# Kernel optimization log

Measured on AMD Instinct MI355X. Metric: run time of the kernel, lower is better.

## Reference

```python
import jax, jax.numpy as jnp
import numpy as np

B, N, D, H = 4, 256, 32, 512

def setup_inputs() -> dict:
    key = jax.random.key(0)
    ks = jax.random.split(key, 6)
    z = jax.random.normal(ks[0], (B, N, D), dtype=jnp.float32)
    motif_mask = (jax.random.uniform(ks[1], (B, N)) > 0.5).astype(jnp.float32)
    residue_mask = jnp.ones((B, N), dtype=jnp.float32)
    # Linear weights stored as (in, out); scaled like torch default init
    W1 = jax.random.normal(ks[2], (D * D, H), dtype=jnp.float32) / np.sqrt(D * D)
    b1 = jnp.zeros((H,), dtype=jnp.float32)
    W2 = jax.random.normal(ks[3], (H, H // 2), dtype=jnp.float32) / np.sqrt(H)
    b2 = jnp.zeros((H // 2,), dtype=jnp.float32)
    W3 = jax.random.normal(ks[4], (H // 2, 1), dtype=jnp.float32) / np.sqrt(H // 2)
    b3 = jnp.zeros((1,), dtype=jnp.float32)
    return {"z": z, "motif_mask": motif_mask, "residue_mask": residue_mask,
            "W1": W1, "b1": b1, "W2": W2, "b2": b2, "W3": W3, "b3": b3}

def reference(z, motif_mask, residue_mask, W1, b1, W2, b2, W3, b3):
    # kron[b,i,j, a*D+c] = z[b,i,a] * z[b,j,c]; first Linear on kron is the
    # bilinear form z_i^T W1_h z_j -- compute via two matmuls, never
    # materializing the (B,N,N,D^2) tensor.
    d = z.shape[-1]
    W1r = W1.reshape(d, d, -1)                      # (D, D, H); axis0 = z_i dim, axis1 = z_j dim
    tmp = jnp.einsum('bia,ach->bihc', z, W1r)        # (B, N, H, D)
    h1 = jax.nn.relu(jnp.einsum('bihc,bjc->bijh', tmp, z) + b1)  # (B, N, N, H)
    h2 = jax.nn.relu(jnp.einsum('bijh,hk->bijk', h1, W2) + b2)   # (B, N, N, H/2)
    contact_logits = (jnp.einsum('bijk,ko->bijo', h2, W3) + b3)[..., 0]  # (B, N, N)
    outer_mask = motif_mask[:, None, :] * motif_mask[:, :, None]
    contact_logits = contact_logits * outer_mask
    contact_map = jax.nn.sigmoid(contact_logits)
    return (contact_map, contact_logits)
```

## Files before the change

kernel.cpp:

```cpp
#include <hip/hip_runtime.h>
#include <hip/hip_bf16.h>
#include <cstdint>
#include <cstddef>

#define NB 4
#define NN 256
#define DD 32
#define HH 512

typedef __attribute__((ext_vector_type(8))) short short8;
typedef __attribute__((ext_vector_type(4))) float f32x4;
typedef __attribute__((ext_vector_type(16))) float f32x16;

static __device__ __forceinline__ unsigned cvtpk(float a, float b) {
  unsigned r;
  asm("v_cvt_pk_bf16_f32 %0, %1, %2" : "=v"(r) : "v"(a), "v"(b));
  return r;
}
static __device__ __forceinline__ unsigned short f2bf1(float a) {
  return (unsigned short)(cvtpk(a, 0.f) & 0xffffu);
}

static __device__ __forceinline__ short8 pack8(float4 a0, float4 a1) {
  union { unsigned u[4]; short8 s; } r;
  r.u[0] = cvtpk(a0.x, a0.y); r.u[1] = cvtpk(a0.z, a0.w);
  r.u[2] = cvtpk(a1.x, a1.y); r.u[3] = cvtpk(a1.z, a1.w);
  return r.s;
}

__global__ __launch_bounds__(256) void prep(const float* __restrict__ z,
                                            const float* __restrict__ W1,
                                            const float* __restrict__ W2,
                                            unsigned short* __restrict__ W2F,
                                            unsigned short* __restrict__ Tall) {
  const int blk = blockIdx.x;
  const int tid = threadIdx.x;
  if (blk < 512) {
    __shared__ unsigned short w1s[16384];
    const int nblk = blk >> 4, mgrp = blk & 15;
    const int bibase = mgrp * 64;

    #pragma unroll
    for (int r = 0; r < 16; ++r) {
      int task = r * 256 + tid;
      int row = task >> 2;
      int hq = task & 3;
      float4 v = *(const float4*)(W1 + (size_t)row * 512 + nblk * 16 + hq * 4);
      int a = row >> 5, c = row & 31;
      int quad = a >> 3, e = a & 7;
      float hv[4] = {v.x, v.y, v.z, v.w};
      #pragma unroll
      for (int vv = 0; vv < 4; ++vv) {
        int hl = hq * 4 + vv;
        int nl = hl * 32 + c;
        int w2 = nl >> 7, r7 = nl & 127;
        int l16 = r7 >> 3, nt = r7 & 7;
        w1s[((w2 * 8 + nt) * 64 + quad * 16 + l16) * 8 + e] = f2bf1(hv[vv]);
      }
    }
    __syncthreads();

    const int w2 = tid >> 6, lane = tid & 63;
    const int quad = lane >> 4, l16 = lane & 15;

    short8 bfr[8];
    #pragma unroll
    for (int nt = 0; nt < 8; ++nt)
      bfr[nt] = *(const short8*)&w1s[((w2 * 8 + nt) * 64 + lane) * 8];

    const int ncol = nblk * 512 + w2 * 128 + l16 * 8;
    #pragma unroll
    for (int mtg = 0; mtg < 2; ++mtg) {
      short8 afr[2];
      #pragma unroll
      for (int mi = 0; mi < 2; ++mi) {
        const float* zr = z + (size_t)(bibase + (mtg * 2 + mi) * 16 + l16) * 32 + quad * 8;
        float4 a0 = *(const float4*)(zr);
        float4 a1 = *(const float4*)(zr + 4);
        afr[mi] = pack8(a0, a1);
      }
      f32x4 d[2][8];
      #pragma unroll
      for (int mi = 0; mi < 2; ++mi)
        #pragma unroll
        for (int nt = 0; nt < 8; ++nt)
          d[mi][nt] = __builtin_amdgcn_mfma_f32_16x16x32_bf16(
              afr[mi], bfr[nt], (f32x4){0.f, 0.f, 0.f, 0.f}, 0, 0, 0);
      #pragma unroll
      for (int mi = 0; mi < 2; ++mi)
        #pragma unroll
        for (int r = 0; r < 4; ++r) {
          size_t rowoff = (size_t)(bibase + (mtg * 2 + mi) * 16 + quad * 4 + r) * 16384;
          uint4 p;
          p.x = cvtpk(d[mi][0][r], d[mi][1][r]);
          p.y = cvtpk(d[mi][2][r], d[mi][3][r]);
          p.z = cvtpk(d[mi][4][r], d[mi][5][r]);
          p.w = cvtpk(d[mi][6][r], d[mi][7][r]);
          *(uint4*)&Tall[rowoff + ncol] = p;
        }
    }
  } else {
    int f8 = (blk - 512) * 256 + tid;
    int lane = f8 & 63;
    int nt = (f8 >> 6) & 1, s = (f8 >> 7) & 3, hc = (f8 >> 9) & 7, w = (f8 >> 12) & 3;
    int k2 = w * 64 + nt * 32 + (lane & 31);
    int hb = hc * 64 + s * 16 + (lane >> 5) * 8;
    float v[8];
    #pragma unroll
    for (int e = 0; e < 8; ++e) v[e] = W2[(hb + e) * 256 + k2];
    uint4 p;
    p.x = cvtpk(v[0], v[1]); p.y = cvtpk(v[2], v[3]);
    p.z = cvtpk(v[4], v[5]); p.w = cvtpk(v[6], v[7]);
    ((uint4*)W2F)[f8] = p;
  }
}

__global__ __launch_bounds__(256) void fused(const unsigned short* __restrict__ Tall,
                                             const unsigned short* __restrict__ W2F,
                                             const float* __restrict__ z,
                                             const float* __restrict__ b1,
                                             const float* __restrict__ b2,
                                             const float* __restrict__ W3,
                                             const float* __restrict__ b3,
                                             const float* __restrict__ motif,
                                             float* __restrict__ out) {
  __shared__ unsigned short h1s[64 * 264];
  __shared__ float red[256];

  const int tid = threadIdx.x;
  const int w = tid >> 6, lane = tid & 63;
  const int quad = lane >> 4, l16 = lane & 15;
  const int L = lane >> 5, c32 = lane & 31;

  const int bx = blockIdx.x;
  const int jt = (bx >> 3) & 3;
  const int bi = (bx & 7) | ((bx >> 5) << 3);
  const int b = bi >> 8, i = bi & 255;
  const int jbase = jt * 64;

  const float mi = motif[bi];
  if (mi == 0.f) {
    if (tid < 64) {
      size_t idx = (size_t)bi * 256 + jbase + tid;
      out[idx] = 0.5f;
      out[(size_t)NB * NN * NN + idx] = 0.f;
    }
    return;
  }

  short8 zfr[4];
  #pragma unroll
  for (int nt = 0; nt < 4; ++nt) {
    const float* zr = z + (size_t)(b * 256 + jbase + nt * 16 + l16) * 32 + quad * 8;
    float4 a0 = *(const float4*)(zr);
    float4 a1 = *(const float4*)(zr + 4);
    zfr[nt] = pack8(a0, a1);
  }

  float b2v[2], w3v[2];
  #pragma unroll
  for (int nt = 0; nt < 2; ++nt) {
    int k2 = w * 64 + nt * 32 + c32;
    b2v[nt] = b2[k2];
    w3v[nt] = W3[k2];
  }

  f32x16 acc[2][2];
  #pragma unroll
  for (int mt = 0; mt < 2; ++mt)
    #pragma unroll
    for (int nt = 0; nt < 2; ++nt)
      acc[mt][nt] = (f32x16){0.f,0.f,0.f,0.f,0.f,0.f,0.f,0.f,
                             0.f,0.f,0.f,0.f,0.f,0.f,0.f,0.f};

  const unsigned short* Tbase = Tall + (size_t)bi * 16384 + (w * 16 + l16) * 32 + quad * 8;
  const unsigned short* Wp = W2F + w * 32768 + lane * 8;
  const float* b1base = b1 + w * 16 + quad * 4;

  #pragma unroll
  for (int half = 0; half < 2; ++half) {
    short8 tfr[4];
    #pragma unroll
    for (int q = 0; q < 4; ++q)
      tfr[q] = *(const short8*)(Tbase + (half * 4 + q) * 2048);
    #pragma unroll
    for (int q = 0; q < 4; ++q) {
      float4 b1f = *(const float4*)(b1base + (half * 4 + q) * 64);
      f32x4 cin = {b1f.x, b1f.y, b1f.z, b1f.w};
      #pragma unroll
      for (int nt = 0; nt < 4; ++nt) {
        f32x4 d = __builtin_amdgcn_mfma_f32_16x16x32_bf16(tfr[q], zfr[nt], cin, 0, 0, 0);
        uint2 p;
        p.x = cvtpk(fmaxf(d[0], 0.f), fmaxf(d[1], 0.f));
        p.y = cvtpk(fmaxf(d[2], 0.f), fmaxf(d[3], 0.f));
        *(uint2*)&h1s[(nt * 16 + l16) * 264 + q * 64 + w * 16 + quad * 4] = p;
      }
    }
    __syncthreads();

    const unsigned short* Wh = Wp + half * 16384;
    const unsigned short* h1r = &h1s[c32 * 264 + L * 8];
    short8 bfp[3][2], afp[2][2];
    #pragma unroll
    for (int p = 0; p < 3; ++p) {
      bfp[p][0] = *(const short8*)(Wh + p * 1024);
      bfp[p][1] = *(const short8*)(Wh + p * 1024 + 512);
    }
    afp[0][0] = *(const short8*)(h1r);
    afp[0][1] = *(const short8*)(h1r + 32 * 264);
    afp[1][0] = *(const short8*)(h1r + 16);
    afp[1][1] = *(const short8*)(h1r + 32 * 264 + 16);
    #pragma unroll
    for (int u = 0; u < 16; ++u) {
      const int cur = u & 1, bq = u % 3;
      short8 a0 = afp[cur][0], a1 = afp[cur][1];
      short8 b0 = bfp[bq][0], b1q = bfp[bq][1];
      if (u < 14) {
        afp[cur][0] = *(const short8*)(h1r + (u + 2) * 16);
        afp[cur][1] = *(const short8*)(h1r + 32 * 264 + (u + 2) * 16);
      }
      if (u < 13) {
        bfp[bq][0] = *(const short8*)(Wh + (u + 3) * 1024);
        bfp[bq][1] = *(const short8*)(Wh + (u + 3) * 1024 + 512);
      }
      acc[0][0] = __builtin_amdgcn_mfma_f32_32x32x16_bf16(a0, b0, acc[0][0], 0, 0, 0);
      acc[0][1] = __builtin_amdgcn_mfma_f32_32x32x16_bf16(a0, b1q, acc[0][1], 0, 0, 0);
      acc[1][0] = __builtin_amdgcn_mfma_f32_32x32x16_bf16(a1, b0, acc[1][0], 0, 0, 0);
      acc[1][1] = __builtin_amdgcn_mfma_f32_32x32x16_bf16(a1, b1q, acc[1][1], 0, 0, 0);
    }
    if (half == 0) __syncthreads();
  }

  float pr[2][16];
  #pragma unroll
  for (int mt = 0; mt < 2; ++mt)
    #pragma unroll
    for (int reg = 0; reg < 16; ++reg) {
      float s = 0.f;
      #pragma unroll
      for (int nt = 0; nt < 2; ++nt) {
        float v = acc[mt][nt][reg] + b2v[nt];
        v = v > 0.f ? v : 0.f;
        s += v * w3v[nt];
      }
      s += __shfl_xor(s, 1);
      s += __shfl_xor(s, 2);
      s += __shfl_xor(s, 4);
      s += __shfl_xor(s, 8);
      s += __shfl_xor(s, 16);
      pr[mt][reg] = s;
    }
  if (c32 == 0) {
    #pragma unroll
    for (int mt = 0; mt < 2; ++mt)
      #pragma unroll
      for (int g = 0; g < 4; ++g) {
        float4 vv = {pr[mt][g * 4 + 0], pr[mt][g * 4 + 1],
                     pr[mt][g * 4 + 2], pr[mt][g * 4 + 3]};
        *(float4*)&red[w * 64 + mt * 32 + g * 8 + L * 4] = vv;
      }
  }
  __syncthreads();
  if (tid < 64) {
    int j = tid;
    float logit = red[j] + red[64 + j] + red[128 + j] + red[192 + j] + b3[0];
    float mm = mi * motif[b * 256 + jbase + j];
    logit *= mm;
    float map = 1.f / (1.f + expf(-logit));
    size_t idx = (size_t)bi * 256 + jbase + j;
    out[idx] = map;
    out[(size_t)NB * NN * NN + idx] = logit;
  }
}

extern "C" void kernel_launch(void* const* d_in, const int* in_sizes, int n_in,
                              void* d_out, int out_size, void* d_ws, size_t ws_size,
                              hipStream_t stream) {
  const float* z     = (const float*)d_in[0];
  const float* motif = (const float*)d_in[1];
  const float* W1 = (const float*)d_in[3];
  const float* b1 = (const float*)d_in[4];
  const float* W2 = (const float*)d_in[5];
  const float* b2 = (const float*)d_in[6];
  const float* W3 = (const float*)d_in[7];
  const float* b3 = (const float*)d_in[8];
  float* out = (float*)d_out;

  char* ws = (char*)d_ws;
  unsigned short* Tall = (unsigned short*)ws;
  unsigned short* W2F  = (unsigned short*)(ws + 33554432);

  prep<<<576, 256, 0, stream>>>(z, W1, W2, W2F, Tall);
  fused<<<4096, 256, 0, stream>>>(Tall, W2F, z, b1, b2, W3, b3, motif, out);
}
```

Before: 146.1 us.

## Compact unmasked j indices per batch to skip masked contact columns

Adds a prep block that uses wave ballots to build, per batch, a compacted list of j positions with nonzero motif mask and a list of masked ones. The fused kernel then processes only live j in 64-wide slot tiles, exits early for tiles beyond the live count, and writes the constant outputs (0.5, 0) for masked j directly. This removes the MLP work for output pairs whose logits are zeroed by the outer mask, at the cost of gathered z loads, scattered output stores and a dependency on per-batch counts.

```diff
diff --git a/kernel.cpp b/kernel.cpp
--- a/kernel.cpp
+++ b/kernel.cpp
@@ -31,8 +31,12 @@
 __global__ __launch_bounds__(256) void prep(const float* __restrict__ z,
                                             const float* __restrict__ W1,
                                             const float* __restrict__ W2,
+                                            const float* __restrict__ motif,
                                             unsigned short* __restrict__ W2F,
-                                            unsigned short* __restrict__ Tall) {
+                                            unsigned short* __restrict__ Tall,
+                                            int* __restrict__ jlist,
+                                            int* __restrict__ mlist,
+                                            int* __restrict__ jcnt) {
   const int blk = blockIdx.x;
   const int tid = threadIdx.x;
   if (blk < 512) {
@@ -99,7 +103,7 @@
           *(uint4*)&Tall[rowoff + ncol] = p;
         }
     }
-  } else {
+  } else if (blk < 576) {
     int f8 = (blk - 512) * 256 + tid;
     int lane = f8 & 63;
     int nt = (f8 >> 6) & 1, s = (f8 >> 7) & 3, hc = (f8 >> 9) & 7, w = (f8 >> 12) & 3;
@@ -112,6 +116,25 @@
     p.x = cvtpk(v[0], v[1]); p.y = cvtpk(v[2], v[3]);
     p.z = cvtpk(v[4], v[5]); p.w = cvtpk(v[6], v[7]);
     ((uint4*)W2F)[f8] = p;
+  } else {
+    const int w = tid >> 6, lane = tid & 63;
+    if (w < NB) {
+      int cnt = 0, mcnt = 0;
+      #pragma unroll
+      for (int ch = 0; ch < 4; ++ch) {
+        int j = ch * 64 + lane;
+        float m = motif[w * 256 + j];
+        bool alive = (m != 0.f);
+        unsigned long long mk = __ballot(alive);
+        unsigned long long below = mk & ((1ull << lane) - 1ull);
+        int pos = __popcll(below);
+        if (alive) jlist[w * 256 + cnt + pos] = j;
+        else       mlist[w * 256 + mcnt + (lane - pos)] = j;
+        int pc = __popcll(mk);
+        cnt += pc; mcnt += 64 - pc;
+      }
+      if (lane == 0) jcnt[w] = cnt;
+    }
   }
 }
 
@@ -123,6 +146,9 @@
                                              const float* __restrict__ W3,
                                              const float* __restrict__ b3,
                                              const float* __restrict__ motif,
+                                             const int* __restrict__ jlist,
+                                             const int* __restrict__ mlist,
+                                             const int* __restrict__ jcnt,
                                              float* __restrict__ out) {
   __shared__ unsigned short h1s[64 * 264];
   __shared__ float red[256];
@@ -135,23 +161,39 @@
   const int bx = blockIdx.x;
   const int jt = (bx >> 3) & 3;
   const int bi = (bx & 7) | ((bx >> 5) << 3);
-  const int b = bi >> 8, i = bi & 255;
-  const int jbase = jt * 64;
-
-  const float mi = motif[bi];
-  if (mi == 0.f) {
+  const int b = bi >> 8;
+  const size_t OUT2 = (size_t)NB * NN * NN;
+
+  const float mi_v = motif[bi];
+  if (mi_v == 0.f) {
     if (tid < 64) {
-      size_t idx = (size_t)bi * 256 + jbase + tid;
+      size_t idx = (size_t)bi * 256 + jt * 64 + tid;
       out[idx] = 0.5f;
-      out[(size_t)NB * NN * NN + idx] = 0.f;
+      out[OUT2 + idx] = 0.f;
     }
     return;
   }
 
+  const int cnt = jcnt[b];
+  if (jt == 0) {
+    int mcnt = 256 - cnt;
+    if (tid < mcnt) {
+      int jm = mlist[b * 256 + tid] & 255;
+      size_t idx = (size_t)bi * 256 + jm;
+      out[idx] = 0.5f;
+      out[OUT2 + idx] = 0.f;
+    }
+  }
+  if (jt * 64 >= cnt) return;
+  const int slotbase = jt * 64;
+
   short8 zfr[4];
   #pragma unroll
   for (int nt = 0; nt < 4; ++nt) {
-    const float* zr = z + (size_t)(b * 256 + jbase + nt * 16 + l16) * 32 + quad * 8;
+    int slot = slotbase + nt * 16 + l16;
+    int sc = slot < cnt ? slot : cnt - 1;
+    int jj = jlist[b * 256 + sc] & 255;
+    const float* zr = z + (size_t)(b * 256 + jj) * 32 + quad * 8;
     float4 a0 = *(const float4*)(zr);
     float4 a1 = *(const float4*)(zr + 4);
     zfr[nt] = pack8(a0, a1);
@@ -262,14 +304,17 @@
   }
   __syncthreads();
   if (tid < 64) {
-    int j = tid;
-    float logit = red[j] + red[64 + j] + red[128 + j] + red[192 + j] + b3[0];
-    float mm = mi * motif[b * 256 + jbase + j];
-    logit *= mm;
-    float map = 1.f / (1.f + expf(-logit));
-    size_t idx = (size_t)bi * 256 + jbase + j;
-    out[idx] = map;
-    out[(size_t)NB * NN * NN + idx] = logit;
+    int slot = slotbase + tid;
+    if (slot < cnt) {
+      int j = jlist[b * 256 + slot] & 255;
+      float logit = red[tid] + red[64 + tid] + red[128 + tid] + red[192 + tid] + b3[0];
+      float mm = mi_v * motif[b * 256 + j];
+      logit *= mm;
+      float map = 1.f / (1.f + expf(-logit));
+      size_t idx = (size_t)bi * 256 + j;
+      out[idx] = map;
+      out[OUT2 + idx] = logit;
+    }
   }
 }
 
@@ -289,7 +334,11 @@
   char* ws = (char*)d_ws;
   unsigned short* Tall = (unsigned short*)ws;
   unsigned short* W2F  = (unsigned short*)(ws + 33554432);
-
-  prep<<<576, 256, 0, stream>>>(z, W1, W2, W2F, Tall);
-  fused<<<4096, 256, 0, stream>>>(Tall, W2F, z, b1, b2, W3, b3, motif, out);
-}
+  int* jlist = (int*)(ws + 33554432 + 262144);
+  int* mlist = (int*)(ws + 33554432 + 262144 + 4096);
+  int* jcnt  = (int*)(ws + 33554432 + 262144 + 8192);
+
+  prep<<<577, 256, 0, stream>>>(z, W1, W2, motif, W2F, Tall, jlist, mlist, jcnt);
+  fused<<<4096, 256, 0, stream>>>(Tall, W2F, z, b1, b2, W3, b3, motif,
+                                  jlist, mlist, jcnt, out);
+}
```

Result: no change. 143.5 us (-1.7%).
